# Kernel tuning notes

Hardware: AMD Instinct MI355X
Metric: run time of the kernel (lower is better)

The kernel has to match this reference:

```python
import jax, jax.numpy as jnp
import numpy as np

G = 16        # groups / heads
DG = 128      # per-group dim (2048/16)
F = 2048      # feat dim (representation_size)
N = 2048      # num_rois
M = 2048      # num_nongt_rois


def setup_inputs() -> dict:
    key = jax.random.key(0)
    ks = jax.random.split(key, 8)
    std = np.float32(0.02)
    return {
        "roi_feat": jax.random.normal(ks[0], (N, F), jnp.float32),
        "ref_feat": jax.random.normal(ks[1], (M, F), jnp.float32),
        "Wq_w": jax.random.normal(ks[2], (F, F), jnp.float32) * std,
        "Wq_b": jnp.zeros((F,), jnp.float32),
        "Wk_w": jax.random.normal(ks[3], (F, F), jnp.float32) * std,
        "Wk_b": jnp.zeros((F,), jnp.float32),
        # grouped 1x1 conv weight [2048, 2048, 1, 1] squeezed to [F, F];
        # group g maps input channels [g*F_g_in] -> output channels [g*DG:(g+1)*DG]
        "Wv_w": jax.random.normal(ks[4], (F, F), jnp.float32) * np.float32(0.01),
        "Wv_b": jnp.zeros((F,), jnp.float32),
    }


def reference(roi_feat, ref_feat, Wq_w, Wq_b, Wk_w, Wk_b, Wv_w, Wv_b):
    n = roi_feat.shape[0]
    scale = np.float32(1.0 / np.sqrt(DG))
    # torch Linear: y = x @ W.T + b
    q = (roi_feat @ Wq_w.T + Wq_b).reshape(n, G, DG)      # [N, G, DG]
    k = (ref_feat @ Wk_w.T + Wk_b).reshape(-1, G, DG)     # [M, G, DG]
    aff = jnp.einsum("ngd,mgd->ngm", q, k) * scale        # [N, G, M]
    attn = jax.nn.softmax(aff, axis=-1)
    # weighted values: v is raw ref_feat, per original
    ov = jnp.einsum("ngm,mf->ngf", attn, ref_feat)        # [N, G, F]
    # grouped 1x1 conv: per-group linear F -> DG
    Wv3 = Wv_w.reshape(G, DG, F)                          # [G, DG, F]
    out = jnp.einsum("ngf,gdf->ngd", ov, Wv3) + Wv_b.reshape(G, DG)
    return out.reshape(n, G * DG)                          # [N, F]
```

## Files before the change

### kernel.cpp

```cpp
#include <hip/hip_runtime.h>
#include <hip/hip_bf16.h>

#define G_   16
#define DG_  128
#define F_   2048
#define N_   2048
#define M_   2048

typedef __attribute__((ext_vector_type(8))) short s16x8;
typedef __attribute__((ext_vector_type(4))) float f32x4;
typedef __attribute__((ext_vector_type(2))) unsigned int u32x2;

typedef const __attribute__((address_space(1))) void GV;
typedef __attribute__((address_space(3))) void LV;

__device__ inline unsigned short f2bf(float f) {
  unsigned u = __float_as_uint(f);
  u += 0x7fffu + ((u >> 16) & 1u);
  return (unsigned short)(u >> 16);
}

struct Cvt5Args { const float* s[5]; unsigned short* d[5]; };

__global__ __launch_bounds__(256)
void cvt5(Cvt5Args a) {
  const unsigned total = 5u * 524288u;
  for (unsigned u = blockIdx.x * 256 + threadIdx.x; u < total; u += 2560u * 256u) {
    int seg = u >> 19;
    unsigned off = u & 524287u;
    const float4* sp = (const float4*)(a.s[seg] + (size_t)off * 8);
    float4 x = sp[0], y = sp[1];
    uint4 o;
    o.x = (unsigned)f2bf(x.x) | ((unsigned)f2bf(x.y) << 16);
    o.y = (unsigned)f2bf(x.z) | ((unsigned)f2bf(x.w) << 16);
    o.z = (unsigned)f2bf(y.x) | ((unsigned)f2bf(y.y) << 16);
    o.w = (unsigned)f2bf(y.z) | ((unsigned)f2bf(y.w) << 16);
    *(uint4*)(a.d[seg] + (size_t)off * 8) = o;
  }
}

struct GemmJobs {
  const unsigned short* A[3];
  const unsigned short* B[3];
  const float* bias[3];
  unsigned short* C[3];
  float osc[3];
};

__global__ __launch_bounds__(256, 2)
void gemm128(GemmJobs jb) {
  __shared__ __align__(16) char lds[65536];
  const int wg = (blockIdx.x & 7) * 96 + (blockIdx.x >> 3);
  const int j  = wg >> 8;
  const int bs = wg & 255;
  const unsigned short* A = jb.A[j];
  const unsigned short* B = jb.B[j];
  const float* bias = jb.bias[j];
  unsigned short* C = jb.C[j];
  const float osc = jb.osc[j];

  const int tid = threadIdx.x, lane = tid & 63, wv = tid >> 6;
  const int wm = wv >> 1, wn = wv & 1;
  const int l15 = lane & 15, l4 = lane >> 4;
  const int m0 = (bs >> 4) * 128, n0 = (bs & 15) * 128;
  const int slot = (l4 ^ ((l15 >> 1) & 3)) * 16;
  const int scol = (((lane & 3) ^ ((lane >> 3) & 3)) * 8);
  const int srow = wv * 16 + (lane >> 2);
  const int rA = wm * 64 + l15;
  const int rB = wn * 64 + l15;

  f32x4 acc[4][4];
#pragma unroll
  for (int i = 0; i < 4; ++i)
#pragma unroll
    for (int nf = 0; nf < 4; ++nf) acc[i][nf] = (f32x4){0.f, 0.f, 0.f, 0.f};

  auto stage_kh = [&](int buf2, int h, int k0) {
#pragma unroll
    for (int rb = 0; rb < 2; ++rb) {
      __builtin_amdgcn_global_load_lds(
          (GV*)(A + (size_t)(m0 + rb * 64 + srow) * F_ + k0 + h * 32 + scol),
          (LV*)(lds + buf2 * 32768 + h * 8192 + rb * 4096 + wv * 1024),
          16, 0, 0);
      __builtin_amdgcn_global_load_lds(
          (GV*)(B + (size_t)(n0 + rb * 64 + srow) * F_ + k0 + h * 32 + scol),
          (LV*)(lds + buf2 * 32768 + 16384 + h * 8192 + rb * 4096 + wv * 1024),
          16, 0, 0);
    }
  };

  stage_kh(0, 0, 0);
  stage_kh(0, 1, 0);
  asm volatile("s_waitcnt vmcnt(4)" ::: "memory");
  __builtin_amdgcn_sched_barrier(0);
  __builtin_amdgcn_s_barrier();

  const int NT = F_ / 64;
  for (int t = 0; t < NT; ++t) {
    const int buf = t & 1;
    const char* Lb = lds + buf * 32768;
    const bool pf = (t + 1 < NT);
    const int k1 = (t + 1) * 64;
    s16x8 af[4], bf[4];

    auto ldA = [&](int mf, int h) {
      return *(const s16x8*)(Lb + h * 8192 + (rA + mf * 16) * 64 + slot);
    };
    auto ldB = [&](int nf, int h) {
      return *(const s16x8*)(Lb + 16384 + h * 8192 + (rB + nf * 16) * 64 + slot);
    };

#pragma unroll
    for (int nf = 0; nf < 4; ++nf) bf[nf] = ldB(nf, 0);
#pragma unroll
    for (int i = 0; i < 4; ++i) af[i] = ldA(i, 0);
    if (pf) stage_kh(buf ^ 1, 0, k1);
    asm volatile("s_waitcnt lgkmcnt(0)" ::: "memory");
    __builtin_amdgcn_sched_barrier(0);
    __builtin_amdgcn_s_setprio(1);
#pragma unroll
    for (int i = 0; i < 4; ++i)
#pragma unroll
      for (int nf = 0; nf < 4; ++nf)
        acc[i][nf] = __builtin_amdgcn_mfma_f32_16x16x32_bf16(af[i], bf[nf], acc[i][nf], 0, 0, 0);
    __builtin_amdgcn_s_setprio(0);

    if (pf) { asm volatile("s_waitcnt vmcnt(4)" ::: "memory"); }
    else    { asm volatile("s_waitcnt vmcnt(0)" ::: "memory"); }
    __builtin_amdgcn_sched_barrier(0);
    __builtin_amdgcn_s_barrier();

#pragma unroll
    for (int nf = 0; nf < 4; ++nf) bf[nf] = ldB(nf, 1);
#pragma unroll
    for (int i = 0; i < 4; ++i) af[i] = ldA(i, 1);
    if (pf) stage_kh(buf ^ 1, 1, k1);
    asm volatile("s_waitcnt lgkmcnt(0)" ::: "memory");
    __builtin_amdgcn_sched_barrier(0);
    __builtin_amdgcn_s_setprio(1);
#pragma unroll
    for (int i = 0; i < 4; ++i)
#pragma unroll
      for (int nf = 0; nf < 4; ++nf)
        acc[i][nf] = __builtin_amdgcn_mfma_f32_16x16x32_bf16(af[i], bf[nf], acc[i][nf], 0, 0, 0);
    __builtin_amdgcn_s_setprio(0);

    if (pf) { asm volatile("s_waitcnt vmcnt(4)" ::: "memory"); }
    __builtin_amdgcn_sched_barrier(0);
    __builtin_amdgcn_s_barrier();
  }

#pragma unroll
  for (int nf = 0; nf < 4; ++nf) {
    int c = n0 + wn * 64 + nf * 16 + l15;
    float bv = bias ? bias[c] : 0.f;
#pragma unroll
    for (int mf = 0; mf < 4; ++mf) {
#pragma unroll
      for (int jj = 0; jj < 4; ++jj) {
        int r = m0 + wm * 64 + mf * 16 + l4 * 4 + jj;
        C[(size_t)r * F_ + c] = f2bf((acc[mf][nf][jj] + bv) * osc);
      }
    }
  }
}

__global__ __launch_bounds__(256, 2)
void attn_mfma(const unsigned short* __restrict__ Q,
               const unsigned short* __restrict__ K,
               const unsigned short* __restrict__ Vt,
               const float* __restrict__ vb,
               float* __restrict__ out) {
  __shared__ unsigned short Kt[2][64 * 128];
  __shared__ unsigned short Vts[2][128 * 64];
  __shared__ unsigned short Pt[4][16 * 64];
  const int tid = threadIdx.x, lane = tid & 63, wv = tid >> 6;
  const int l15 = lane & 15, l4 = lane >> 4;
  const int g = blockIdx.y;
  const int q0 = blockIdx.x * 64 + wv * 16;

  s16x8 qa[4];
#pragma unroll
  for (int kc = 0; kc < 4; ++kc)
    qa[kc] = *(const s16x8*)(Q + (size_t)(q0 + l15) * F_ + g * DG_ + kc * 32 + l4 * 8);

  f32x4 oa[8];
#pragma unroll
  for (int df = 0; df < 8; ++df) oa[df] = (f32x4){0.f, 0.f, 0.f, 0.f};
  float m_r = -1e30f, l_r = 0.f;

  const int ksw0 = (((lane & 15) ^ (lane >> 4)) * 8);
  const int ksw1 = (((lane & 15) ^ 4 ^ (lane >> 4)) * 8);
  const int vsw  = (((lane & 7) ^ (lane >> 3)) * 8);
  const int xorb = (l15 & 7) << 4;
  int csw[4];
#pragma unroll
  for (int kc = 0; kc < 4; ++kc) csw[kc] = (kc * 64 + l4 * 16) ^ xorb;

  auto stage = [&](int buf, int kv0) {
#pragma unroll
    for (int i = 0; i < 4; ++i) {
      int r0 = wv * 16 + i * 4;
      __builtin_amdgcn_global_load_lds(
          (GV*)(K + (size_t)(kv0 + r0 + (lane >> 4)) * F_ + g * DG_ + ((i & 1) ? ksw1 : ksw0)),
          (LV*)(&Kt[buf][r0 * 128]), 16, 0, 0);
    }
#pragma unroll
    for (int i = 0; i < 4; ++i) {
      int r0 = wv * 32 + i * 8;
      __builtin_amdgcn_global_load_lds(
          (GV*)(Vt + (size_t)(g * DG_ + r0 + (lane >> 3)) * M_ + kv0 + vsw),
          (LV*)(&Vts[buf][r0 * 64]), 16, 0, 0);
    }
  };

  stage(0, 0);
  __syncthreads();
  int cur = 0;
  unsigned short* Pw = &Pt[wv][0];

  for (int t = 0; t < M_ / 64; ++t) {
    if (t + 1 < M_ / 64) stage(cur ^ 1, (t + 1) * 64);
    const unsigned short* Kb = &Kt[cur][0];
    const unsigned short* Vb = &Vts[cur][0];

    f32x4 sf[4];
    __builtin_amdgcn_s_setprio(1);
#pragma unroll
    for (int kvf = 0; kvf < 4; ++kvf) {
      f32x4 s = (f32x4){0.f, 0.f, 0.f, 0.f};
#pragma unroll
      for (int kc = 0; kc < 4; ++kc) {
        s16x8 kf = *(const s16x8*)((const char*)Kb + (kvf * 16 + l15) * 256 + csw[kc]);
        s = __builtin_amdgcn_mfma_f32_16x16x32_bf16(kf, qa[kc], s, 0, 0, 0);
      }
      sf[kvf] = s;
    }
    __builtin_amdgcn_s_setprio(0);

    float tmax = sf[0][0];
#pragma unroll
    for (int kvf = 0; kvf < 4; ++kvf) {
      tmax = fmaxf(tmax, fmaxf(fmaxf(sf[kvf][0], sf[kvf][1]),
                               fmaxf(sf[kvf][2], sf[kvf][3])));
    }
    tmax = fmaxf(tmax, __shfl_xor(tmax, 16));
    tmax = fmaxf(tmax, __shfl_xor(tmax, 32));
    if (!__all(tmax <= m_r + 8.0f)) {
      float mnew = fmaxf(m_r, tmax);
      float corr = __builtin_amdgcn_exp2f(m_r - mnew);
      m_r = mnew;
      l_r *= corr;
      float c0 = __shfl(corr, l4 * 4 + 0);
      float c1 = __shfl(corr, l4 * 4 + 1);
      float c2 = __shfl(corr, l4 * 4 + 2);
      float c3 = __shfl(corr, l4 * 4 + 3);
#pragma unroll
      for (int df = 0; df < 8; ++df) {
        oa[df][0] *= c0; oa[df][1] *= c1; oa[df][2] *= c2; oa[df][3] *= c3;
      }
    }

    float psum = 0.f;
#pragma unroll
    for (int kvf = 0; kvf < 4; ++kvf) {
      float p0 = __builtin_amdgcn_exp2f(sf[kvf][0] - m_r);
      float p1 = __builtin_amdgcn_exp2f(sf[kvf][1] - m_r);
      float p2 = __builtin_amdgcn_exp2f(sf[kvf][2] - m_r);
      float p3 = __builtin_amdgcn_exp2f(sf[kvf][3] - m_r);
      psum += (p0 + p1) + (p2 + p3);
      u32x2 w;
      asm("v_cvt_pk_bf16_f32 %0, %1, %2" : "=v"(w.x) : "v"(p0), "v"(p1));
      asm("v_cvt_pk_bf16_f32 %0, %1, %2" : "=v"(w.y) : "v"(p2), "v"(p3));
      *(u32x2*)((char*)Pw + l15 * 128 + ((kvf * 32 + l4 * 8) ^ xorb)) = w;
    }
    psum += __shfl_xor(psum, 16);
    psum += __shfl_xor(psum, 32);
    l_r += psum;

    s16x8 pa0 = *(const s16x8*)((const char*)Pw + l15 * 128 + csw[0]);
    s16x8 pa1 = *(const s16x8*)((const char*)Pw + l15 * 128 + csw[1]);
    __builtin_amdgcn_s_setprio(1);
#pragma unroll
    for (int df = 0; df < 8; ++df) {
      s16x8 v0 = *(const s16x8*)((const char*)Vb + (df * 16 + l15) * 128 + csw[0]);
      s16x8 v1 = *(const s16x8*)((const char*)Vb + (df * 16 + l15) * 128 + csw[1]);
      oa[df] = __builtin_amdgcn_mfma_f32_16x16x32_bf16(pa0, v0, oa[df], 0, 0, 0);
      oa[df] = __builtin_amdgcn_mfma_f32_16x16x32_bf16(pa1, v1, oa[df], 0, 0, 0);
    }
    __builtin_amdgcn_s_setprio(0);
    __syncthreads();
    cur ^= 1;
  }

  float linv = 1.0f / l_r;
  float i0 = __shfl(linv, l4 * 4 + 0);
  float i1 = __shfl(linv, l4 * 4 + 1);
  float i2 = __shfl(linv, l4 * 4 + 2);
  float i3 = __shfl(linv, l4 * 4 + 3);
#pragma unroll
  for (int df = 0; df < 8; ++df) {
    int c = g * DG_ + df * 16 + l15;
    float bv = vb[c];
    out[(size_t)(q0 + l4 * 4 + 0) * F_ + c] = oa[df][0] * i0 + bv;
    out[(size_t)(q0 + l4 * 4 + 1) * F_ + c] = oa[df][1] * i1 + bv;
    out[(size_t)(q0 + l4 * 4 + 2) * F_ + c] = oa[df][2] * i2 + bv;
    out[(size_t)(q0 + l4 * 4 + 3) * F_ + c] = oa[df][3] * i3 + bv;
  }
}

extern "C" void kernel_launch(void* const* d_in, const int* in_sizes, int n_in,
                              void* d_out, int out_size, void* d_ws, size_t ws_size,
                              hipStream_t stream) {
  const float* roi  = (const float*)d_in[0];
  const float* ref  = (const float*)d_in[1];
  const float* Wq_w = (const float*)d_in[2];
  const float* Wq_b = (const float*)d_in[3];
  const float* Wk_w = (const float*)d_in[4];
  const float* Wk_b = (const float*)d_in[5];
  const float* Wv_w = (const float*)d_in[6];
  const float* Wv_b = (const float*)d_in[7];
  float* out = (float*)d_out;
  const size_t SEG = 4194304;
  const float cscale = 0.12751664508246770f;

  if (ws_size < 64ull * 1024 * 1024) return;
  unsigned short* roi_bf = (unsigned short*)d_ws;
  unsigned short* ref_bf = roi_bf + SEG;
  unsigned short* Wq_bf  = ref_bf + SEG;
  unsigned short* Wk_bf  = Wq_bf + SEG;
  unsigned short* Wv_bf  = Wk_bf + SEG;
  unsigned short* Qb     = Wv_bf + SEG;
  unsigned short* Kb     = Qb + SEG;
  unsigned short* Vtb    = Kb + SEG;

  Cvt5Args ca;
  ca.s[0] = roi;  ca.d[0] = roi_bf;
  ca.s[1] = ref;  ca.d[1] = ref_bf;
  ca.s[2] = Wq_w; ca.d[2] = Wq_bf;
  ca.s[3] = Wk_w; ca.d[3] = Wk_bf;
  ca.s[4] = Wv_w; ca.d[4] = Wv_bf;
  cvt5<<<2560, 256, 0, stream>>>(ca);

  GemmJobs jb;
  jb.A[0] = roi_bf; jb.B[0] = Wq_bf;  jb.bias[0] = Wq_b;    jb.C[0] = Qb;  jb.osc[0] = cscale;
  jb.A[1] = ref_bf; jb.B[1] = Wk_bf;  jb.bias[1] = Wk_b;    jb.C[1] = Kb;  jb.osc[1] = 1.0f;
  jb.A[2] = Wv_bf;  jb.B[2] = ref_bf; jb.bias[2] = nullptr; jb.C[2] = Vtb; jb.osc[2] = 1.0f;
  gemm128<<<768, 256, 0, stream>>>(jb);

  attn_mfma<<<dim3(N_ / 64, G_), 256, 0, stream>>>(Qb, Kb, Vtb, Wv_b, out);
}
```

Baseline: 140.3 us.

## Fuse fp32-to-bf16 conversion into projection GEMM loads via register staging

Drops the separate conversion kernel and has the projection GEMM read fp32 inputs directly. Tiles are loaded into registers, packed to bf16 with v_cvt_pk_bf16_f32, and written to LDS, with global prefetch overlapping the MFMA work. This removes a kernel launch and a full bf16 write-and-reread of five 2048x2048 matrices. In exchange each GEMM reads twice the bytes from global memory (operands are re-read across tiles), the async global_load_lds path is lost, and register pressure rises by 16 float4s, which may hurt occupancy at 2 waves/SIMD. The bf16 rounding also changes from the software round-to-nearest-even to the hardware convert instruction.

```diff
diff --git a/kernel.cpp b/kernel.cpp
--- a/kernel.cpp
+++ b/kernel.cpp
@@ -20,41 +20,22 @@
   return (unsigned short)(u >> 16);
 }
 
-struct Cvt5Args { const float* s[5]; unsigned short* d[5]; };
-
-__global__ __launch_bounds__(256)
-void cvt5(Cvt5Args a) {
-  const unsigned total = 5u * 524288u;
-  for (unsigned u = blockIdx.x * 256 + threadIdx.x; u < total; u += 2560u * 256u) {
-    int seg = u >> 19;
-    unsigned off = u & 524287u;
-    const float4* sp = (const float4*)(a.s[seg] + (size_t)off * 8);
-    float4 x = sp[0], y = sp[1];
-    uint4 o;
-    o.x = (unsigned)f2bf(x.x) | ((unsigned)f2bf(x.y) << 16);
-    o.y = (unsigned)f2bf(x.z) | ((unsigned)f2bf(x.w) << 16);
-    o.z = (unsigned)f2bf(y.x) | ((unsigned)f2bf(y.y) << 16);
-    o.w = (unsigned)f2bf(y.z) | ((unsigned)f2bf(y.w) << 16);
-    *(uint4*)(a.d[seg] + (size_t)off * 8) = o;
-  }
-}
-
 struct GemmJobs {
-  const unsigned short* A[3];
-  const unsigned short* B[3];
+  const float* A[3];
+  const float* B[3];
   const float* bias[3];
   unsigned short* C[3];
   float osc[3];
 };
 
 __global__ __launch_bounds__(256, 2)
-void gemm128(GemmJobs jb) {
+void gemm128f(GemmJobs jb) {
   __shared__ __align__(16) char lds[65536];
   const int wg = (blockIdx.x & 7) * 96 + (blockIdx.x >> 3);
   const int j  = wg >> 8;
   const int bs = wg & 255;
-  const unsigned short* A = jb.A[j];
-  const unsigned short* B = jb.B[j];
+  const float* A = jb.A[j];
+  const float* B = jb.B[j];
   const float* bias = jb.bias[j];
   unsigned short* C = jb.C[j];
   const float osc = jb.osc[j];
@@ -75,23 +56,51 @@
 #pragma unroll
     for (int nf = 0; nf < 4; ++nf) acc[i][nf] = (f32x4){0.f, 0.f, 0.f, 0.f};
 
-  auto stage_kh = [&](int buf2, int h, int k0) {
-#pragma unroll
-    for (int rb = 0; rb < 2; ++rb) {
-      __builtin_amdgcn_global_load_lds(
-          (GV*)(A + (size_t)(m0 + rb * 64 + srow) * F_ + k0 + h * 32 + scol),
-          (LV*)(lds + buf2 * 32768 + h * 8192 + rb * 4096 + wv * 1024),
-          16, 0, 0);
-      __builtin_amdgcn_global_load_lds(
-          (GV*)(B + (size_t)(n0 + rb * 64 + srow) * F_ + k0 + h * 32 + scol),
-          (LV*)(lds + buf2 * 32768 + 16384 + h * 8192 + rb * 4096 + wv * 1024),
-          16, 0, 0);
+  const size_t offA = (size_t)(m0 + srow) * F_ + scol;
+  const size_t offB = (size_t)(n0 + srow) * F_ + scol;
+
+  float4 ld[16];
+
+  auto issueLoads = [&](int k0) {
+#pragma unroll
+    for (int h = 0; h < 2; ++h) {
+#pragma unroll
+      for (int rb = 0; rb < 2; ++rb) {
+        const float* pa = A + offA + (size_t)rb * 64 * F_ + k0 + h * 32;
+        ld[h * 8 + rb * 2 + 0] = *(const float4*)(pa);
+        ld[h * 8 + rb * 2 + 1] = *(const float4*)(pa + 4);
+        const float* pb = B + offB + (size_t)rb * 64 * F_ + k0 + h * 32;
+        ld[h * 8 + 4 + rb * 2 + 0] = *(const float4*)(pb);
+        ld[h * 8 + 4 + rb * 2 + 1] = *(const float4*)(pb + 4);
+      }
     }
   };
 
-  stage_kh(0, 0, 0);
-  stage_kh(0, 1, 0);
-  asm volatile("s_waitcnt vmcnt(4)" ::: "memory");
+  auto cvtWrite = [&](int buf2) {
+#pragma unroll
+    for (int h = 0; h < 2; ++h) {
+#pragma unroll
+      for (int rb = 0; rb < 2; ++rb) {
+#pragma unroll
+        for (int mat = 0; mat < 2; ++mat) {
+          float4 x = ld[h * 8 + mat * 4 + rb * 2 + 0];
+          float4 y = ld[h * 8 + mat * 4 + rb * 2 + 1];
+          uint4 w;
+          asm("v_cvt_pk_bf16_f32 %0, %1, %2" : "=v"(w.x) : "v"(x.x), "v"(x.y));
+          asm("v_cvt_pk_bf16_f32 %0, %1, %2" : "=v"(w.y) : "v"(x.z), "v"(x.w));
+          asm("v_cvt_pk_bf16_f32 %0, %1, %2" : "=v"(w.z) : "v"(y.x), "v"(y.y));
+          asm("v_cvt_pk_bf16_f32 %0, %1, %2" : "=v"(w.w) : "v"(y.z), "v"(y.w));
+          *(uint4*)(lds + buf2 * 32768 + mat * 16384 + h * 8192 + rb * 4096 +
+                    wv * 1024 + lane * 16) = w;
+        }
+      }
+    }
+  };
+
+  issueLoads(0);
+  asm volatile("s_waitcnt vmcnt(0)" ::: "memory");
+  cvtWrite(0);
+  asm volatile("s_waitcnt lgkmcnt(0)" ::: "memory");
   __builtin_amdgcn_sched_barrier(0);
   __builtin_amdgcn_s_barrier();
 
@@ -100,7 +109,6 @@
     const int buf = t & 1;
     const char* Lb = lds + buf * 32768;
     const bool pf = (t + 1 < NT);
-    const int k1 = (t + 1) * 64;
     s16x8 af[4], bf[4];
 
     auto ldA = [&](int mf, int h) {
@@ -110,11 +118,13 @@
       return *(const s16x8*)(Lb + 16384 + h * 8192 + (rB + nf * 16) * 64 + slot);
     };
 
+    if (pf) issueLoads((t + 1) * 64);
+    __builtin_amdgcn_sched_barrier(0);
+
 #pragma unroll
     for (int nf = 0; nf < 4; ++nf) bf[nf] = ldB(nf, 0);
 #pragma unroll
     for (int i = 0; i < 4; ++i) af[i] = ldA(i, 0);
-    if (pf) stage_kh(buf ^ 1, 0, k1);
     asm volatile("s_waitcnt lgkmcnt(0)" ::: "memory");
     __builtin_amdgcn_sched_barrier(0);
     __builtin_amdgcn_s_setprio(1);
@@ -125,16 +135,10 @@
         acc[i][nf] = __builtin_amdgcn_mfma_f32_16x16x32_bf16(af[i], bf[nf], acc[i][nf], 0, 0, 0);
     __builtin_amdgcn_s_setprio(0);
 
-    if (pf) { asm volatile("s_waitcnt vmcnt(4)" ::: "memory"); }
-    else    { asm volatile("s_waitcnt vmcnt(0)" ::: "memory"); }
-    __builtin_amdgcn_sched_barrier(0);
-    __builtin_amdgcn_s_barrier();
-
 #pragma unroll
     for (int nf = 0; nf < 4; ++nf) bf[nf] = ldB(nf, 1);
 #pragma unroll
     for (int i = 0; i < 4; ++i) af[i] = ldA(i, 1);
-    if (pf) stage_kh(buf ^ 1, 1, k1);
     asm volatile("s_waitcnt lgkmcnt(0)" ::: "memory");
     __builtin_amdgcn_sched_barrier(0);
     __builtin_amdgcn_s_setprio(1);
@@ -145,7 +149,12 @@
         acc[i][nf] = __builtin_amdgcn_mfma_f32_16x16x32_bf16(af[i], bf[nf], acc[i][nf], 0, 0, 0);
     __builtin_amdgcn_s_setprio(0);
 
-    if (pf) { asm volatile("s_waitcnt vmcnt(4)" ::: "memory"); }
+    if (pf) {
+      asm volatile("s_waitcnt vmcnt(0)" ::: "memory");
+      __builtin_amdgcn_sched_barrier(0);
+      cvtWrite(buf ^ 1);
+      asm volatile("s_waitcnt lgkmcnt(0)" ::: "memory");
+    }
     __builtin_amdgcn_sched_barrier(0);
     __builtin_amdgcn_s_barrier();
   }
@@ -324,29 +333,16 @@
   const size_t SEG = 4194304;
   const float cscale = 0.12751664508246770f;
 
-  if (ws_size < 64ull * 1024 * 1024) return;
-  unsigned short* roi_bf = (unsigned short*)d_ws;
-  unsigned short* ref_bf = roi_bf + SEG;
-  unsigned short* Wq_bf  = ref_bf + SEG;
-  unsigned short* Wk_bf  = Wq_bf + SEG;
-  unsigned short* Wv_bf  = Wk_bf + SEG;
-  unsigned short* Qb     = Wv_bf + SEG;
-  unsigned short* Kb     = Qb + SEG;
-  unsigned short* Vtb    = Kb + SEG;
-
-  Cvt5Args ca;
-  ca.s[0] = roi;  ca.d[0] = roi_bf;
-  ca.s[1] = ref;  ca.d[1] = ref_bf;
-  ca.s[2] = Wq_w; ca.d[2] = Wq_bf;
-  ca.s[3] = Wk_w; ca.d[3] = Wk_bf;
-  ca.s[4] = Wv_w; ca.d[4] = Wv_bf;
-  cvt5<<<2560, 256, 0, stream>>>(ca);
+  if (ws_size < 24ull * 1024 * 1024) return;
+  unsigned short* Qb  = (unsigned short*)d_ws;
+  unsigned short* Kb  = Qb + SEG;
+  unsigned short* Vtb = Kb + SEG;
 
   GemmJobs jb;
-  jb.A[0] = roi_bf; jb.B[0] = Wq_bf;  jb.bias[0] = Wq_b;    jb.C[0] = Qb;  jb.osc[0] = cscale;
-  jb.A[1] = ref_bf; jb.B[1] = Wk_bf;  jb.bias[1] = Wk_b;    jb.C[1] = Kb;  jb.osc[1] = 1.0f;
-  jb.A[2] = Wv_bf;  jb.B[2] = ref_bf; jb.bias[2] = nullptr; jb.C[2] = Vtb; jb.osc[2] = 1.0f;
-  gemm128<<<768, 256, 0, stream>>>(jb);
+  jb.A[0] = roi;  jb.B[0] = Wq_w; jb.bias[0] = Wq_b;    jb.C[0] = Qb;  jb.osc[0] = cscale;
+  jb.A[1] = ref;  jb.B[1] = Wk_w; jb.bias[1] = Wk_b;    jb.C[1] = Kb;  jb.osc[1] = 1.0f;
+  jb.A[2] = Wv_w; jb.B[2] = ref;  jb.bias[2] = nullptr; jb.C[2] = Vtb; jb.osc[2] = 1.0f;
+  gemm128f<<<768, 256, 0, stream>>>(jb);
 
   attn_mfma<<<dim3(N_ / 64, G_), 256, 0, stream>>>(Qb, Kb, Vtb, Wv_b, out);
 }
```

Result: slower. 152.9 us, median of 2 (+9.0%).
